# Optimization experiments

Measured on AMD Instinct MI355X. Metric: run time of the kernel, lower is better.

Reference implementation:

```python
import jax, jax.numpy as jnp
import numpy as np

N = 50000
E = 800000
IN_DIM = 128
HEADS = 4
OUT_DIM = 32
TOT = HEADS * OUT_DIM  # 128 == IN_DIM -> residual_proj is None
LN_EPS = 1e-5
NEG_SLOPE = 0.2


def setup_inputs() -> dict:
    key = jax.random.key(0)
    ks = jax.random.split(key, 10)
    x = jax.random.normal(ks[0], (N, IN_DIM), dtype=jnp.float32)
    # random edges guaranteed src != dst (PyG GATv2Conv removes then re-adds self loops)
    src = jax.random.randint(ks[1], (E,), 0, N)
    off = jax.random.randint(ks[2], (E,), 1, N)
    dst = (src + off) % N
    edge_index = jnp.stack([src, dst]).astype(jnp.int64)
    # glorot-style init for weights
    sc = 1.0 / np.sqrt(IN_DIM)
    W_l = jax.random.uniform(ks[3], (IN_DIM, TOT), jnp.float32, -sc, sc)
    b_l = jnp.zeros((TOT,), jnp.float32)
    W_r = jax.random.uniform(ks[4], (IN_DIM, TOT), jnp.float32, -sc, sc)
    b_r = jnp.zeros((TOT,), jnp.float32)
    att = jax.random.uniform(ks[5], (HEADS, OUT_DIM), jnp.float32, -sc, sc)
    bias = jnp.zeros((TOT,), jnp.float32)
    ln_g = jnp.ones((TOT,), jnp.float32)
    ln_b = jnp.zeros((TOT,), jnp.float32)
    return {"x": x, "edge_index": edge_index, "W_l": W_l, "b_l": b_l,
            "W_r": W_r, "b_r": b_r, "att": att, "bias": bias,
            "ln_g": ln_g, "ln_b": ln_b}


def _gatv2_layer(x, src, dst, W_l, b_l, W_r, b_r, att, bias, ln_g, ln_b):
    n = x.shape[0]
    # GATv2Conv: x_l = lin_l(x) (source/messages), x_r = lin_r(x) (target)
    xl = (x @ W_l + b_l).reshape(n, HEADS, OUT_DIM)
    xr = (x @ W_r + b_r).reshape(n, HEADS, OUT_DIM)
    m = xl[src] + xr[dst]                               # [E+N, H, D]
    s = jnp.einsum('ehd,hd->eh', jax.nn.leaky_relu(m, NEG_SLOPE), att)
    # per-destination softmax (every node has a self loop -> no empty segments)
    smax = jax.ops.segment_max(s, dst, num_segments=n)  # [N, H]
    e = jnp.exp(s - smax[dst])
    denom = jax.ops.segment_sum(e, dst, num_segments=n)
    alpha = e / denom[dst]                              # [E+N, H]
    out = jax.ops.segment_sum(alpha[..., None] * xl[src], dst, num_segments=n)
    out = out.reshape(n, TOT) + bias
    out = out + x                                       # residual (in_dim == total_out_dim)
    mu = jnp.mean(out, axis=-1, keepdims=True)
    var = jnp.mean(jnp.square(out - mu), axis=-1, keepdims=True)
    y = (out - mu) / jnp.sqrt(var + LN_EPS) * ln_g + ln_b
    return jax.nn.elu(y)


def reference(x, edge_index, W_l, b_l, W_r, b_r, att, bias, ln_g, ln_b):
    n = x.shape[0]
    loops = jnp.arange(n, dtype=edge_index.dtype)
    src = jnp.concatenate([edge_index[0], loops])
    dst = jnp.concatenate([edge_index[1], loops])
    return _gatv2_layer(x, src, dst, W_l, b_l, W_r, b_r, att, bias, ln_g, ln_b)
```

## Files before the change

kernel.cpp:

```cpp
#include <hip/hip_runtime.h>

#define N_NODES 50000
#define E_EDGES 800000
#define M_TOTAL (E_EDGES + N_NODES)
#define IN_DIM 128
#define HEADS 4
#define OUT_DIM 32
#define TOT 128
#define LN_EPS 1e-5f
#define NEG_SLOPE 0.2f

#define SCAN_NBLK ((N_NODES + 255) / 256)
#define GEMM_NBLK ((N_NODES + 63) / 64)
#define MBLOCKS ((M_TOTAL + 255) / 256)
#define ZERO_NBLK ((8 * N_NODES / 4 + 255) / 256)

typedef __bf16 bf16x8 __attribute__((ext_vector_type(8)));
typedef float  f32x4  __attribute__((ext_vector_type(4)));
typedef _Float16 h2   __attribute__((ext_vector_type(2)));

__device__ __forceinline__ float quad_sum(float p) {
    p += __int_as_float(__builtin_amdgcn_update_dpp(
        0, __float_as_int(p), 0xB1 , 0xF, 0xF, true));
    p += __int_as_float(__builtin_amdgcn_update_dpp(
        0, __float_as_int(p), 0x4E , 0xF, 0xF, true));
    return p;
}

__global__ __launch_bounds__(256) void init_kernel(
    const float* __restrict__ Wl, const float* __restrict__ Wr,
    unsigned* __restrict__ WT, int* __restrict__ deg8) {
    const int b = blockIdx.x, t = threadIdx.x;
    if (b < 64) {
        const int u = b * 256 + t;
        const int col = u >> 6, k2 = u & 63;
        const float* __restrict__ W = (col < 128) ? Wl : Wr;
        const int c = col & 127;
        union { __bf16 bb[2]; unsigned uu; } p;
        p.bb[0] = (__bf16)W[(2 * k2) * TOT + c];
        p.bb[1] = (__bf16)W[(2 * k2 + 1) * TOT + c];
        WT[col * 64 + k2] = p.uu;
    } else {
        const int i = (b - 64) * 256 + t;
        if (i < 8 * N_NODES / 4) ((int4*)deg8)[i] = make_int4(0, 0, 0, 0);
    }
}

__global__ __launch_bounds__(256) void histgemm_kernel(
    const int* __restrict__ dsts, int* __restrict__ deg8,
    unsigned char* __restrict__ rank8,
    const float* __restrict__ x, const unsigned* __restrict__ WT,
    const float* __restrict__ bl, const float* __restrict__ br,
    unsigned* __restrict__ xlb, unsigned* __restrict__ xrb) {
    if (blockIdx.x >= GEMM_NBLK) {
        const int hb = blockIdx.x - GEMM_NBLK;
        const int m = hb * 256 + threadIdx.x;
        if (m >= M_TOTAL) return;
        const int d = (m < E_EDGES) ? dsts[m] : (m - E_EDGES);
        const int shard = hb & 7;
        rank8[m] = (unsigned char)atomicAdd(&deg8[shard * N_NODES + d], 1);
        return;
    }
    __shared__ float epi[4][16][66];
    const int t = threadIdx.x, w = t >> 6, lane = t & 63;
    const int q = lane >> 4, ln = lane & 15;
    const int m0 = blockIdx.x * 64;

    const int row = min(m0 + w * 16 + ln, N_NODES - 1);
    const float* __restrict__ xrow = x + (size_t)row * IN_DIM;
    bf16x8 A[4];
#pragma unroll
    for (int c = 0; c < 4; ++c) {
        const float4 v0 = *(const float4*)&xrow[c * 32 + q * 8];
        const float4 v1 = *(const float4*)&xrow[c * 32 + q * 8 + 4];
        bf16x8 a;
        a[0] = (__bf16)v0.x; a[1] = (__bf16)v0.y; a[2] = (__bf16)v0.z; a[3] = (__bf16)v0.w;
        a[4] = (__bf16)v1.x; a[5] = (__bf16)v1.y; a[6] = (__bf16)v1.z; a[7] = (__bf16)v1.w;
        A[c] = a;
    }

    const int mr = lane >> 2, cg2 = (lane & 3) * 16;
    const int grow = m0 + w * 16 + mr;
#pragma unroll
    for (int g = 0; g < 4; ++g) {
        const int n0 = g * 64;
        const float* __restrict__ bvec = (g < 2) ? bl : br;
        f32x4 acc[4];
#pragma unroll
        for (int nt = 0; nt < 4; ++nt) {
            const float b = bvec[(n0 & 127) + nt * 16 + ln];
            acc[nt] = (f32x4){b, b, b, b};
        }
#pragma unroll
        for (int nt = 0; nt < 4; ++nt) {
            const int col = n0 + nt * 16 + ln;
#pragma unroll
            for (int c = 0; c < 4; ++c) {
                const bf16x8 B = *(const bf16x8*)&WT[col * 64 + c * 16 + q * 4];
                acc[nt] = __builtin_amdgcn_mfma_f32_16x16x32_bf16(A[c], B, acc[nt], 0, 0, 0);
            }
        }
#pragma unroll
        for (int nt = 0; nt < 4; ++nt)
#pragma unroll
            for (int r = 0; r < 4; ++r)
                epi[w][q * 4 + r][nt * 16 + ln] = acc[nt][r];

        if (grow < N_NODES) {
            unsigned p[8];
#pragma unroll
            for (int i = 0; i < 8; ++i) {
                union { _Float16 h[2]; unsigned u; } pk;
                pk.h[0] = (_Float16)epi[w][mr][cg2 + 2 * i];
                pk.h[1] = (_Float16)epi[w][mr][cg2 + 2 * i + 1];
                p[i] = pk.u;
            }
            unsigned* __restrict__ dst = ((g < 2) ? xlb : xrb) +
                (size_t)grow * 64 + (g & 1) * 32 + (cg2 >> 1);
            *(uint4*)&dst[0] = make_uint4(p[0], p[1], p[2], p[3]);
            *(uint4*)&dst[4] = make_uint4(p[4], p[5], p[6], p[7]);
        }
    }
}

__global__ __launch_bounds__(256) void scan1_kernel(
    const int* __restrict__ deg8, unsigned char* __restrict__ base8,
    int* __restrict__ incl, int* __restrict__ blockSums,
    int* __restrict__ degtot) {
    __shared__ int sh[256];
    const int t = threadIdx.x;
    const int i = blockIdx.x * 256 + t;
    int tot = 0;
    if (i < N_NODES) {
        int run = 0;
#pragma unroll
        for (int s = 0; s < 8; ++s) {
            base8[s * N_NODES + i] = (unsigned char)run;
            run += deg8[s * N_NODES + i];
        }
        tot = run;
        degtot[i] = tot;
    }
    sh[t] = tot;
    __syncthreads();
#pragma unroll
    for (int off = 1; off < 256; off <<= 1) {
        int u = (t >= off) ? sh[t - off] : 0;
        __syncthreads();
        sh[t] += u;
        __syncthreads();
    }
    if (i < N_NODES) incl[i] = sh[t];
    if (t == 255) blockSums[blockIdx.x] = sh[255];
}

__global__ __launch_bounds__(256) void scan23_kernel(
    const int* __restrict__ degtot, const int* __restrict__ blockSums,
    int* __restrict__ rowptr ) {
    __shared__ int sh[256];
    const int t = threadIdx.x;
    const int v0 = (t < SCAN_NBLK) ? blockSums[t] : 0;
    sh[t] = v0;
    __syncthreads();
#pragma unroll
    for (int off = 1; off < 256; off <<= 1) {
        int u = (t >= off) ? sh[t - off] : 0;
        __syncthreads();
        sh[t] += u;
        __syncthreads();
    }
    const int blockOff = (blockIdx.x == 0) ? 0 : sh[blockIdx.x - 1];
    const int i = blockIdx.x * 256 + t;
    if (i < N_NODES)
        rowptr[i] = blockOff + rowptr[i] - degtot[i];
    if (i == 0) rowptr[N_NODES] = M_TOTAL;
}

__global__ __launch_bounds__(256) void scatter_kernel(
    const int* __restrict__ srcs, const int* __restrict__ dsts,
    const int* __restrict__ rowptr, const unsigned char* __restrict__ base8,
    const unsigned char* __restrict__ rank8,
    unsigned short* __restrict__ sorted16) {
    const int b = blockIdx.x;
    const int m = b * 256 + threadIdx.x;
    if (m >= M_TOTAL) return;
    int s, d;
    if (m < E_EDGES) { s = srcs[m]; d = dsts[m]; }
    else             { s = d = m - E_EDGES; }
    const int shard = b & 7;
    const int pos = rowptr[d] + (int)base8[shard * N_NODES + d] + (int)rank8[m];
    sorted16[pos] = (unsigned short)s;
}

__global__ __launch_bounds__(256) void gat_kernel(
    const int* __restrict__ rowptr, const unsigned short* __restrict__ sorted16,
    const unsigned* __restrict__ xlb, const unsigned* __restrict__ xrb,
    const float* __restrict__ att, const float* __restrict__ x,
    const float* __restrict__ bias, const float* __restrict__ g,
    const float* __restrict__ bvec, float* __restrict__ out) {
    const int d = blockIdx.x * 4 + (threadIdx.x >> 6);
    const int lane = threadIdx.x & 63;
    const int ln = lane & 15, q = lane >> 4;
    if (d >= N_NODES) return;

    h2 xrh[4], ath[4];
    {
        const uint4 ur = *(const uint4*)&xrb[(size_t)d * 64 + 4 * ln];
        union { uint4 u; h2 h[4]; } cr; cr.u = ur;
        xrh[0] = cr.h[0]; xrh[1] = cr.h[1]; xrh[2] = cr.h[2]; xrh[3] = cr.h[3];
        const float4 a0 = *(const float4*)&att[8 * ln];
        const float4 a1 = *(const float4*)&att[8 * ln + 4];
        ath[0][0] = (_Float16)a0.x; ath[0][1] = (_Float16)a0.y;
        ath[1][0] = (_Float16)a0.z; ath[1][1] = (_Float16)a0.w;
        ath[2][0] = (_Float16)a1.x; ath[2][1] = (_Float16)a1.y;
        ath[3][0] = (_Float16)a1.z; ath[3][1] = (_Float16)a1.w;
    }
    const h2 slope = (h2){(_Float16)NEG_SLOPE, (_Float16)NEG_SLOPE};
    const int beg = rowptr[d], end = rowptr[d + 1];

    float l = 0.f;
    float acc[8];
#pragma unroll
    for (int k = 0; k < 8; ++k) acc[k] = 0.f;

    int s_b = (int)sorted16[min(beg + 4 + q, end - 1)];
    uint4 u;
    {
        const int s_a = (int)sorted16[min(beg + q, end - 1)];
        u = *(const uint4*)&xlb[(size_t)s_a * 64 + 4 * ln];
    }

    for (int base = beg; base < end; base += 4) {
        const int s_c = (int)sorted16[min(base + 8 + q, end - 1)];
        const uint4 u_next = *(const uint4*)&xlb[(size_t)s_b * 64 + 4 * ln];

        const bool valid = (base + q) < end;
        union { unsigned uu; h2 h; } c0, c1, c2, c3;
        c0.uu = u.x; c1.uu = u.y; c2.uu = u.z; c3.uu = u.w;
        h2 m0 = c0.h + xrh[0], m1 = c1.h + xrh[1];
        h2 m2 = c2.h + xrh[2], m3 = c3.h + xrh[3];
        m0 = __builtin_elementwise_max(m0, m0 * slope);
        m1 = __builtin_elementwise_max(m1, m1 * slope);
        m2 = __builtin_elementwise_max(m2, m2 * slope);
        m3 = __builtin_elementwise_max(m3, m3 * slope);
        float p = __builtin_amdgcn_fdot2(m0, ath[0], 0.0f, false);
        p = __builtin_amdgcn_fdot2(m1, ath[1], p, false);
        p = __builtin_amdgcn_fdot2(m2, ath[2], p, false);
        p = __builtin_amdgcn_fdot2(m3, ath[3], p, false);
        p = quad_sum(p);
        const float e = valid ? __expf(p) : 0.f;
        l += e;
        acc[0] = fmaf(e, (float)c0.h[0], acc[0]);
        acc[1] = fmaf(e, (float)c0.h[1], acc[1]);
        acc[2] = fmaf(e, (float)c1.h[0], acc[2]);
        acc[3] = fmaf(e, (float)c1.h[1], acc[3]);
        acc[4] = fmaf(e, (float)c2.h[0], acc[4]);
        acc[5] = fmaf(e, (float)c2.h[1], acc[5]);
        acc[6] = fmaf(e, (float)c3.h[0], acc[6]);
        acc[7] = fmaf(e, (float)c3.h[1], acc[7]);

        u = u_next; s_b = s_c;
    }

#pragma unroll
    for (int off = 16; off <= 32; off <<= 1) {
        l += __shfl_xor(l, off, 64);
#pragma unroll
        for (int k = 0; k < 8; ++k) acc[k] += __shfl_xor(acc[k], off, 64);
    }

    const float inv_l = 1.0f / l;
    const float4 xv0 = *(const float4*)&x[(size_t)d * TOT + 8 * ln];
    const float4 xv1 = *(const float4*)&x[(size_t)d * TOT + 8 * ln + 4];
    const float4 bi0 = *(const float4*)&bias[8 * ln];
    const float4 bi1 = *(const float4*)&bias[8 * ln + 4];
    float v[8];
    v[0] = fmaf(acc[0], inv_l, bi0.x + xv0.x);
    v[1] = fmaf(acc[1], inv_l, bi0.y + xv0.y);
    v[2] = fmaf(acc[2], inv_l, bi0.z + xv0.z);
    v[3] = fmaf(acc[3], inv_l, bi0.w + xv0.w);
    v[4] = fmaf(acc[4], inv_l, bi1.x + xv1.x);
    v[5] = fmaf(acc[5], inv_l, bi1.y + xv1.y);
    v[6] = fmaf(acc[6], inv_l, bi1.z + xv1.z);
    v[7] = fmaf(acc[7], inv_l, bi1.w + xv1.w);
    float sum = 0.f, sq = 0.f;
#pragma unroll
    for (int k = 0; k < 8; ++k) { sum += v[k]; sq = fmaf(v[k], v[k], sq); }
#pragma unroll
    for (int off = 1; off <= 8; off <<= 1) {
        sum += __shfl_xor(sum, off, 64);
        sq  += __shfl_xor(sq,  off, 64);
    }
    const float mu  = sum * (1.0f / TOT);
    const float var = sq * (1.0f / TOT) - mu * mu;
    const float inv = rsqrtf(var + LN_EPS);
    const float4 g0 = *(const float4*)&g[8 * ln];
    const float4 g1 = *(const float4*)&g[8 * ln + 4];
    const float4 b0 = *(const float4*)&bvec[8 * ln];
    const float4 b1 = *(const float4*)&bvec[8 * ln + 4];
    float y[8];
    y[0] = (v[0] - mu) * inv * g0.x + b0.x;
    y[1] = (v[1] - mu) * inv * g0.y + b0.y;
    y[2] = (v[2] - mu) * inv * g0.z + b0.z;
    y[3] = (v[3] - mu) * inv * g0.w + b0.w;
    y[4] = (v[4] - mu) * inv * g1.x + b1.x;
    y[5] = (v[5] - mu) * inv * g1.y + b1.y;
    y[6] = (v[6] - mu) * inv * g1.z + b1.z;
    y[7] = (v[7] - mu) * inv * g1.w + b1.w;
#pragma unroll
    for (int k = 0; k < 8; ++k) y[k] = y[k] > 0.f ? y[k] : __expf(y[k]) - 1.f;
    if (q < 2) {
        float4 o = (q == 0) ? make_float4(y[0], y[1], y[2], y[3])
                            : make_float4(y[4], y[5], y[6], y[7]);
        *(float4*)&out[(size_t)d * TOT + 8 * ln + 4 * q] = o;
    }
}

extern "C" void kernel_launch(void* const* d_in, const int* in_sizes, int n_in,
                              void* d_out, int out_size, void* d_ws, size_t ws_size,
                              hipStream_t stream) {
    const float* x    = (const float*)d_in[0];
    const int*   ei   = (const int*)d_in[1];
    const float* Wl   = (const float*)d_in[2];
    const float* bl   = (const float*)d_in[3];
    const float* Wr   = (const float*)d_in[4];
    const float* br   = (const float*)d_in[5];
    const float* att  = (const float*)d_in[6];
    const float* bias = (const float*)d_in[7];
    const float* ln_g = (const float*)d_in[8];
    const float* ln_b = (const float*)d_in[9];
    const int* srcs = ei;
    const int* dsts = ei + E_EDGES;

    unsigned* xlb = (unsigned*)d_ws;
    unsigned* xrb = xlb + (size_t)N_NODES * 64;
    int*   deg8       = (int*)(xrb + (size_t)N_NODES * 64);
    int*   degtot     = deg8 + 8 * N_NODES;
    int*   rowptr     = degtot + N_NODES;
    int*   blockSums  = rowptr + N_NODES + 1;
    unsigned* WT      = (unsigned*)(blockSums + SCAN_NBLK);
    unsigned short* sorted16 = (unsigned short*)(WT + 256 * 64);
    unsigned char*  base8    = (unsigned char*)(sorted16 + M_TOTAL);
    unsigned char*  rank8    = base8 + 8 * N_NODES;

    init_kernel<<<64 + ZERO_NBLK, 256, 0, stream>>>(Wl, Wr, WT, deg8);
    histgemm_kernel<<<GEMM_NBLK + MBLOCKS, 256, 0, stream>>>(
        dsts, deg8, rank8, x, WT, bl, br, xlb, xrb);
    scan1_kernel<<<SCAN_NBLK, 256, 0, stream>>>(deg8, base8, rowptr, blockSums, degtot);
    scan23_kernel<<<SCAN_NBLK, 256, 0, stream>>>(degtot, blockSums, rowptr);
    scatter_kernel<<<MBLOCKS, 256, 0, stream>>>(srcs, dsts, rowptr, base8, rank8, sorted16);
    gat_kernel<<<(N_NODES + 3) / 4, 256, 0, stream>>>(rowptr, sorted16, xlb, xrb, att, x,
                                                      bias, ln_g, ln_b, (float*)d_out);
}
```

Measured before the change: 202.8 us.

## Process four edges per thread in histogram/scatter and accumulate messages in fp16

The histogram and scatter phases now handle four consecutive edges per thread, using vectorized int4 loads of src/dst and uchar4 loads and stores of ranks. Shard assignment changes to edge-index based (m0>>8)&7 so the histogram and scatter phases stay consistent. In the GAT aggregation loop, the weighted message sum is accumulated in packed fp16 with h2 FMAs instead of eight fp32 FMAs, and is reduced through shuffles on packed values. This cuts ALU work and register use, but fp16 accumulation of exp weights risks overflow and precision loss for high-degree nodes, since values are not max-subtracted.

```diff
diff --git a/kernel.cpp b/kernel.cpp
--- a/kernel.cpp
+++ b/kernel.cpp
@@ -12,7 +12,7 @@
 
 #define SCAN_NBLK ((N_NODES + 255) / 256)
 #define GEMM_NBLK ((N_NODES + 63) / 64)
-#define MBLOCKS ((M_TOTAL + 255) / 256)
+#define CHUNK_NBLK ((M_TOTAL / 4 + 255) / 256)
 #define ZERO_NBLK ((8 * N_NODES / 4 + 255) / 256)
 
 typedef __bf16 bf16x8 __attribute__((ext_vector_type(8)));
@@ -54,11 +54,23 @@
     unsigned* __restrict__ xlb, unsigned* __restrict__ xrb) {
     if (blockIdx.x >= GEMM_NBLK) {
         const int hb = blockIdx.x - GEMM_NBLK;
-        const int m = hb * 256 + threadIdx.x;
-        if (m >= M_TOTAL) return;
-        const int d = (m < E_EDGES) ? dsts[m] : (m - E_EDGES);
-        const int shard = hb & 7;
-        rank8[m] = (unsigned char)atomicAdd(&deg8[shard * N_NODES + d], 1);
+        const int m0 = (hb * 256 + threadIdx.x) * 4;
+        if (m0 >= M_TOTAL) return;
+        int d[4];
+        if (m0 < E_EDGES) {
+            const int4 dv = *(const int4*)&dsts[m0];
+            d[0] = dv.x; d[1] = dv.y; d[2] = dv.z; d[3] = dv.w;
+        } else {
+            d[0] = m0 - E_EDGES; d[1] = d[0] + 1; d[2] = d[0] + 2; d[3] = d[0] + 3;
+        }
+        const int shard = (m0 >> 8) & 7;
+        int* __restrict__ cnt = deg8 + shard * N_NODES;
+        uchar4 r;
+        r.x = (unsigned char)atomicAdd(&cnt[d[0]], 1);
+        r.y = (unsigned char)atomicAdd(&cnt[d[1]], 1);
+        r.z = (unsigned char)atomicAdd(&cnt[d[2]], 1);
+        r.w = (unsigned char)atomicAdd(&cnt[d[3]], 1);
+        *(uchar4*)&rank8[m0] = r;
         return;
     }
     __shared__ float epi[4][16][66];
@@ -181,15 +193,29 @@
     const int* __restrict__ rowptr, const unsigned char* __restrict__ base8,
     const unsigned char* __restrict__ rank8,
     unsigned short* __restrict__ sorted16) {
-    const int b = blockIdx.x;
-    const int m = b * 256 + threadIdx.x;
-    if (m >= M_TOTAL) return;
-    int s, d;
-    if (m < E_EDGES) { s = srcs[m]; d = dsts[m]; }
-    else             { s = d = m - E_EDGES; }
-    const int shard = b & 7;
-    const int pos = rowptr[d] + (int)base8[shard * N_NODES + d] + (int)rank8[m];
-    sorted16[pos] = (unsigned short)s;
+    const int m0 = (blockIdx.x * 256 + threadIdx.x) * 4;
+    if (m0 >= M_TOTAL) return;
+    int s[4], d[4];
+    if (m0 < E_EDGES) {
+        const int4 sv = *(const int4*)&srcs[m0];
+        const int4 dv = *(const int4*)&dsts[m0];
+        s[0] = sv.x; s[1] = sv.y; s[2] = sv.z; s[3] = sv.w;
+        d[0] = dv.x; d[1] = dv.y; d[2] = dv.z; d[3] = dv.w;
+    } else {
+        s[0] = d[0] = m0 - E_EDGES;
+        s[1] = d[1] = d[0] + 1; s[2] = d[2] = d[0] + 2; s[3] = d[3] = d[0] + 3;
+    }
+    const int shard = (m0 >> 8) & 7;
+    const unsigned char* __restrict__ bs = base8 + shard * N_NODES;
+    const uchar4 r = *(const uchar4*)&rank8[m0];
+    const int p0 = rowptr[d[0]] + (int)bs[d[0]] + (int)r.x;
+    const int p1 = rowptr[d[1]] + (int)bs[d[1]] + (int)r.y;
+    const int p2 = rowptr[d[2]] + (int)bs[d[2]] + (int)r.z;
+    const int p3 = rowptr[d[3]] + (int)bs[d[3]] + (int)r.w;
+    sorted16[p0] = (unsigned short)s[0];
+    sorted16[p1] = (unsigned short)s[1];
+    sorted16[p2] = (unsigned short)s[2];
+    sorted16[p3] = (unsigned short)s[3];
 }
 
 __global__ __launch_bounds__(256) void gat_kernel(
@@ -219,9 +245,9 @@
     const int beg = rowptr[d], end = rowptr[d + 1];
 
     float l = 0.f;
-    float acc[8];
-#pragma unroll
-    for (int k = 0; k < 8; ++k) acc[k] = 0.f;
+    h2 acc4[4];
+#pragma unroll
+    for (int k = 0; k < 4; ++k) acc4[k] = (h2){(_Float16)0.f, (_Float16)0.f};
 
     int s_b = (int)sorted16[min(beg + 4 + q, end - 1)];
     uint4 u;
@@ -250,14 +276,12 @@
         p = quad_sum(p);
         const float e = valid ? __expf(p) : 0.f;
         l += e;
-        acc[0] = fmaf(e, (float)c0.h[0], acc[0]);
-        acc[1] = fmaf(e, (float)c0.h[1], acc[1]);
-        acc[2] = fmaf(e, (float)c1.h[0], acc[2]);
-        acc[3] = fmaf(e, (float)c1.h[1], acc[3]);
-        acc[4] = fmaf(e, (float)c2.h[0], acc[4]);
-        acc[5] = fmaf(e, (float)c2.h[1], acc[5]);
-        acc[6] = fmaf(e, (float)c3.h[0], acc[6]);
-        acc[7] = fmaf(e, (float)c3.h[1], acc[7]);
+        const _Float16 eh = (_Float16)e;
+        const h2 e2 = (h2){eh, eh};
+        acc4[0] += e2 * c0.h;
+        acc4[1] += e2 * c1.h;
+        acc4[2] += e2 * c2.h;
+        acc4[3] += e2 * c3.h;
 
         u = u_next; s_b = s_c;
     }
@@ -266,7 +290,17 @@
     for (int off = 16; off <= 32; off <<= 1) {
         l += __shfl_xor(l, off, 64);
 #pragma unroll
-        for (int k = 0; k < 8; ++k) acc[k] += __shfl_xor(acc[k], off, 64);
+        for (int k = 0; k < 4; ++k) {
+            union { h2 h; int i; } tmp; tmp.h = acc4[k];
+            tmp.i = __shfl_xor(tmp.i, off, 64);
+            acc4[k] += tmp.h;
+        }
+    }
+    float acc[8];
+#pragma unroll
+    for (int k = 0; k < 4; ++k) {
+        acc[2 * k]     = (float)acc4[k][0];
+        acc[2 * k + 1] = (float)acc4[k][1];
     }
 
     const float inv_l = 1.0f / l;
@@ -344,11 +378,11 @@
     unsigned char*  rank8    = base8 + 8 * N_NODES;
 
     init_kernel<<<64 + ZERO_NBLK, 256, 0, stream>>>(Wl, Wr, WT, deg8);
-    histgemm_kernel<<<GEMM_NBLK + MBLOCKS, 256, 0, stream>>>(
+    histgemm_kernel<<<GEMM_NBLK + CHUNK_NBLK, 256, 0, stream>>>(
         dsts, deg8, rank8, x, WT, bl, br, xlb, xrb);
     scan1_kernel<<<SCAN_NBLK, 256, 0, stream>>>(deg8, base8, rowptr, blockSums, degtot);
     scan23_kernel<<<SCAN_NBLK, 256, 0, stream>>>(degtot, blockSums, rowptr);
-    scatter_kernel<<<MBLOCKS, 256, 0, stream>>>(srcs, dsts, rowptr, base8, rank8, sorted16);
+    scatter_kernel<<<CHUNK_NBLK, 256, 0, stream>>>(srcs, dsts, rowptr, base8, rank8, sorted16);
     gat_kernel<<<(N_NODES + 3) / 4, 256, 0, stream>>>(rowptr, sorted16, xlb, xrb, att, x,
                                                       bias, ln_g, ln_b, (float*)d_out);
 }
```

Result: no change. 206.0 us (+1.6%).
